# Performance work log

Hardware: AMD Instinct MI355X
Metric: run time of the kernel (lower is better)

The kernel has to match this reference:

```python
import jax, jax.numpy as jnp
import numpy as np

D_MODEL = 1024
BATCH = 8
SEQ = 2048
LN_EPS = 1e-5


def setup_inputs() -> dict:
    key = jax.random.key(0)
    ks = jax.random.split(key, 8)
    scale = 0.1 / np.sqrt(D_MODEL)
    x = jax.random.normal(ks[0], (BATCH, SEQ, D_MODEL), dtype=jnp.float32)
    return {
        "x": x,
        "ln_w": jnp.ones((D_MODEL,), jnp.float32),
        "ln_b": jnp.zeros((D_MODEL,), jnp.float32),
        # layer_idx=0, n_layers=4 -> ratio_1 = 1.0 (init), perturb slightly for a non-trivial mix
        "tmk": jnp.ones((D_MODEL,), jnp.float32) * 0.9,
        "tmv": jnp.ones((D_MODEL,), jnp.float32) * 0.9,
        "tmr": jnp.ones((D_MODEL,), jnp.float32) * 0.9,
        "decay_w": jnp.full((D_MODEL,), -0.5, jnp.float32)
        + 0.1 * jax.random.normal(ks[1], (D_MODEL,), jnp.float32),
        "Wk": scale * jax.random.normal(ks[2], (D_MODEL, D_MODEL), jnp.float32),
        "Wv": scale * jax.random.normal(ks[3], (D_MODEL, D_MODEL), jnp.float32),
        "Wr": scale * jax.random.normal(ks[4], (D_MODEL, D_MODEL), jnp.float32),
        "Wo": scale * jax.random.normal(ks[5], (D_MODEL, D_MODEL), jnp.float32),
    }


def _layernorm(z, w, b):
    m = jnp.mean(z, axis=-1, keepdims=True)
    v = jnp.mean(jnp.square(z - m), axis=-1, keepdims=True)
    return (z - m) * jax.lax.rsqrt(v + LN_EPS) * w + b


def reference(x, ln_w, ln_b, tmk, tmv, tmr, decay_w, Wk, Wv, Wr, Wo):
    # x: (B, T, D)
    xn = _layernorm(x, ln_w, ln_b)
    # prev_x at t=0 is zeros (not LN of zeros), afterwards LN(x_{t-1})
    prev = jnp.pad(xn[:, :-1, :], ((0, 0), (1, 0), (0, 0)))
    xk = xn * tmk + prev * (1.0 - tmk)
    xv = xn * tmv + prev * (1.0 - tmv)
    xr = xn * tmr + prev * (1.0 - tmr)
    k = jnp.einsum("btd,ed->bte", xk, Wk)
    v = jnp.einsum("btd,ed->bte", xv, Wv)
    r = jax.nn.sigmoid(jnp.einsum("btd,ed->bte", xr, Wr))
    decay = jax.nn.sigmoid(decay_w)  # (D,)

    kv = (k * v).swapaxes(0, 1)  # (T, B, D) time-major for scan

    def step(S, kv_t):
        S_new = decay * S + kv_t
        return S_new, S_new

    S0 = jnp.zeros((x.shape[0], x.shape[2]), x.dtype)
    final_S, S_seq = jax.lax.scan(step, S0, kv)
    S_seq = S_seq.swapaxes(0, 1)  # (B, T, D)

    out = x + r * jnp.einsum("btd,ed->bte", S_seq, Wo)
    return out, final_S, S_seq
```

## Files before the change

kernel.cpp:

```cpp
#include <hip/hip_runtime.h>
#include <cstdint>

#define D_MODEL 1024
#define SEQ 2048
#define BATCH 8
#define M_TOTAL (BATCH*SEQ)
#define NC 64
#define CL (SEQ/NC)

typedef float f32x4 __attribute__((ext_vector_type(4)));
typedef short bf16x8 __attribute__((ext_vector_type(8)));
typedef unsigned short u16x4 __attribute__((ext_vector_type(4)));

__device__ __forceinline__ float b2f(unsigned short s){
  union { float f; unsigned u; } z; z.u = ((unsigned)s) << 16; return z.f;
}
__device__ __forceinline__ unsigned short f2b(float f){
  union { float f; unsigned u; } z; z.f = f;
  unsigned u = z.u;
  u += 0x7fffu + ((u >> 16) & 1u);
  return (unsigned short)(u >> 16);
}
__device__ __forceinline__ float sigmoidf_(float v){
  return 1.0f / (1.0f + __expf(-v));
}
__device__ __forceinline__ void gld_lds16(const void* g, void* l){
  __builtin_amdgcn_global_load_lds((const __attribute__((address_space(1))) unsigned int*)g,
                                   (__attribute__((address_space(3))) unsigned int*)l,
                                   16, 0, 0);
}

__device__ __forceinline__ void swz256(int bid, int& m0, int& n0){
  int xcd = bid & 7;
  int loc = bid >> 3;
  int wg  = xcd*32 + loc;
  m0 = (wg >> 2) * 256;
  n0 = (wg & 3) * 256;
}

__global__ __launch_bounds__(256) void wconv_kernel(const float* __restrict__ W0, const float* __restrict__ W1,
                                                    const float* __restrict__ W2, const float* __restrict__ W3,
                                                    unsigned short* __restrict__ WC){
  int mat = blockIdx.y;
  const float* src = (mat==0) ? W0 : (mat==1) ? W1 : (mat==2) ? W2 : W3;
  size_t i = ((size_t)blockIdx.x*256 + threadIdx.x)*4;
  f32x4 v = *(const f32x4*)(src + i);
  u16x4 o; o[0]=f2b(v[0]); o[1]=f2b(v[1]); o[2]=f2b(v[2]); o[3]=f2b(v[3]);
  *(u16x4*)(WC + (size_t)mat*1048576 + i) = o;
}

__global__ __launch_bounds__(256) void lnmix_kernel(const float* __restrict__ x,
                                                    const float* __restrict__ lnw, const float* __restrict__ lnb,
                                                    const float* __restrict__ tmk, const float* __restrict__ tmv,
                                                    const float* __restrict__ tmr,
                                                    unsigned short* __restrict__ XK, unsigned short* __restrict__ XV,
                                                    unsigned short* __restrict__ XR){
  int m = blockIdx.x;
  int tid = threadIdx.x;
  bool first = (m & (SEQ-1)) == 0;
  size_t base = (size_t)m*D_MODEL + tid*4;
  f32x4 xc = *(const f32x4*)(x + base);
  f32x4 xp = {0.f,0.f,0.f,0.f};
  if (!first) xp = *(const f32x4*)(x + base - D_MODEL);

  float c1 = xc[0]+xc[1]+xc[2]+xc[3];
  float c2 = xc[0]*xc[0]+xc[1]*xc[1]+xc[2]*xc[2]+xc[3]*xc[3];
  float p1 = xp[0]+xp[1]+xp[2]+xp[3];
  float p2 = xp[0]*xp[0]+xp[1]*xp[1]+xp[2]*xp[2]+xp[3]*xp[3];
  #pragma unroll
  for (int off = 32; off > 0; off >>= 1){
    c1 += __shfl_xor(c1, off); c2 += __shfl_xor(c2, off);
    p1 += __shfl_xor(p1, off); p2 += __shfl_xor(p2, off);
  }
  __shared__ float rc1[4], rc2[4], rp1[4], rp2[4];
  int w = tid >> 6, lane = tid & 63;
  if (lane == 0){ rc1[w]=c1; rc2[w]=c2; rp1[w]=p1; rp2[w]=p2; }
  __syncthreads();
  c1 = rc1[0]+rc1[1]+rc1[2]+rc1[3];
  c2 = rc2[0]+rc2[1]+rc2[2]+rc2[3];
  p1 = rp1[0]+rp1[1]+rp1[2]+rp1[3];
  p2 = rp2[0]+rp2[1]+rp2[2]+rp2[3];
  float mC = c1*(1.0f/1024.0f), vC = c2*(1.0f/1024.0f)-mC*mC, rC = rsqrtf(vC+1e-5f);
  float mP = p1*(1.0f/1024.0f), vP = p2*(1.0f/1024.0f)-mP*mP, rP = rsqrtf(vP+1e-5f);

  f32x4 wv = *(const f32x4*)(lnw + tid*4);
  f32x4 bv = *(const f32x4*)(lnb + tid*4);
  f32x4 k4 = *(const f32x4*)(tmk + tid*4);
  f32x4 v4 = *(const f32x4*)(tmv + tid*4);
  f32x4 r4 = *(const f32x4*)(tmr + tid*4);
  u16x4 ok, ov, orr;
  #pragma unroll
  for (int j=0;j<4;j++){
    float nc = (xc[j]-mC)*rC*wv[j] + bv[j];
    float np = first ? 0.f : (xp[j]-mP)*rP*wv[j] + bv[j];
    ok[j]  = f2b(np + k4[j]*(nc-np));
    ov[j]  = f2b(np + v4[j]*(nc-np));
    orr[j] = f2b(np + r4[j]*(nc-np));
  }
  *(u16x4*)(XK + base) = ok;
  *(u16x4*)(XV + base) = ov;
  *(u16x4*)(XR + base) = orr;
}

__device__ __forceinline__ void gemm256_core(const unsigned short* __restrict__ A,
                                             const unsigned short* __restrict__ W,
                                             int m0, int n0, int tid,
                                             unsigned short* As, unsigned short* Bs,
                                             f32x4 (&acc)[8][4]){
  int wid = tid >> 6, lane = tid & 63;
  int wm = wid >> 2, wn = wid & 3;
  int fr = lane & 15, fg = lane >> 4;

  int offAg[4], offBg[4], offL[4];
  #pragma unroll
  for (int it = 0; it < 4; ++it){
    int chunk = it*512 + tid;
    int row = chunk >> 3;
    int cg = (chunk & 7) ^ (row & 7);
    offAg[it] = (m0+row)*D_MODEL + cg*8;
    offBg[it] = (n0+row)*D_MODEL + cg*8;
    offL[it]  = chunk*8;
  }

  #define STAGE(bsel, kt_) { \
    _Pragma("unroll") \
    for (int it = 0; it < 4; ++it){ \
      gld_lds16(A + offAg[it] + (kt_)*64, &As[(bsel)*16384 + offL[it]]); \
      gld_lds16(W + offBg[it] + (kt_)*64, &Bs[(bsel)*16384 + offL[it]]); \
    } }

  STAGE(0, 0);
  STAGE(1, 1);
  asm volatile("s_waitcnt vmcnt(8)" ::: "memory");
  __builtin_amdgcn_s_barrier();

  bf16x8 aL[4][2], aH[4][2], bL[2][2], bH[2][2];

  #pragma unroll 1
  for (int kt = 0; kt < 16; ++kt){
    const unsigned short* Ab = &As[(kt & 1)*16384];
    const unsigned short* Bb = &Bs[(kt & 1)*16384];

    #pragma unroll
    for (int mi=0; mi<4; ++mi)
      #pragma unroll
      for (int ks=0; ks<2; ++ks){
        int r = wm*128 + mi*16 + fr;
        aL[mi][ks] = *(const bf16x8*)(&Ab[r*64 + (((ks*4+fg)^(r&7))<<3)]);
      }
    #pragma unroll
    for (int ni=0; ni<2; ++ni)
      #pragma unroll
      for (int ks=0; ks<2; ++ks){
        int r = wn*64 + ni*16 + fr;
        bL[ni][ks] = *(const bf16x8*)(&Bb[r*64 + (((ks*4+fg)^(r&7))<<3)]);
      }
    __builtin_amdgcn_s_barrier();
    asm volatile("s_waitcnt lgkmcnt(0)" ::: "memory");
    __builtin_amdgcn_s_setprio(1);
    #pragma unroll
    for (int mi=0; mi<4; ++mi)
      #pragma unroll
      for (int ni=0; ni<2; ++ni)
        #pragma unroll
        for (int ks=0; ks<2; ++ks)
          acc[mi][ni] = __builtin_amdgcn_mfma_f32_16x16x32_bf16(aL[mi][ks], bL[ni][ks], acc[mi][ni], 0, 0, 0);
    __builtin_amdgcn_s_setprio(0);
    __builtin_amdgcn_s_barrier();

    #pragma unroll
    for (int ni=0; ni<2; ++ni)
      #pragma unroll
      for (int ks=0; ks<2; ++ks){
        int r = wn*64 + (ni+2)*16 + fr;
        bH[ni][ks] = *(const bf16x8*)(&Bb[r*64 + (((ks*4+fg)^(r&7))<<3)]);
      }
    __builtin_amdgcn_s_barrier();
    asm volatile("s_waitcnt lgkmcnt(0)" ::: "memory");
    __builtin_amdgcn_s_setprio(1);
    #pragma unroll
    for (int mi=0; mi<4; ++mi)
      #pragma unroll
      for (int ni=0; ni<2; ++ni)
        #pragma unroll
        for (int ks=0; ks<2; ++ks)
          acc[mi][ni+2] = __builtin_amdgcn_mfma_f32_16x16x32_bf16(aL[mi][ks], bH[ni][ks], acc[mi][ni+2], 0, 0, 0);
    __builtin_amdgcn_s_setprio(0);
    __builtin_amdgcn_s_barrier();

    #pragma unroll
    for (int mi=0; mi<4; ++mi)
      #pragma unroll
      for (int ks=0; ks<2; ++ks){
        int r = wm*128 + (mi+4)*16 + fr;
        aH[mi][ks] = *(const bf16x8*)(&Ab[r*64 + (((ks*4+fg)^(r&7))<<3)]);
      }
    asm volatile("s_waitcnt lgkmcnt(0)" ::: "memory");
    __builtin_amdgcn_s_barrier();
    asm volatile("" ::: "memory");
    __builtin_amdgcn_s_setprio(1);
    #pragma unroll
    for (int mi=0; mi<4; ++mi)
      #pragma unroll
      for (int ni=0; ni<2; ++ni)
        #pragma unroll
        for (int ks=0; ks<2; ++ks)
          acc[mi+4][ni+2] = __builtin_amdgcn_mfma_f32_16x16x32_bf16(aH[mi][ks], bH[ni][ks], acc[mi+4][ni+2], 0, 0, 0);
    __builtin_amdgcn_s_setprio(0);

    if (kt < 14) STAGE((kt & 1), kt+2);
    __builtin_amdgcn_s_setprio(1);
    #pragma unroll
    for (int mi=0; mi<4; ++mi)
      #pragma unroll
      for (int ni=0; ni<2; ++ni)
        #pragma unroll
        for (int ks=0; ks<2; ++ks)
          acc[mi+4][ni] = __builtin_amdgcn_mfma_f32_16x16x32_bf16(aH[mi][ks], bL[ni][ks], acc[mi+4][ni], 0, 0, 0);
    __builtin_amdgcn_s_setprio(0);
    if (kt < 14)      asm volatile("s_waitcnt vmcnt(8)" ::: "memory");
    else if (kt == 14) asm volatile("s_waitcnt vmcnt(0)" ::: "memory");
    if (kt < 15){
      __builtin_amdgcn_s_barrier();
      asm volatile("" ::: "memory");
    }
  }
  #undef STAGE
}

__global__ __launch_bounds__(512) void gemm_mix3_kernel(const unsigned short* __restrict__ XK,
                                                        const unsigned short* __restrict__ XV,
                                                        const unsigned short* __restrict__ XR,
                                                        const unsigned short* __restrict__ WC,
                                                        unsigned short* __restrict__ KB,
                                                        unsigned short* __restrict__ VB,
                                                        unsigned short* __restrict__ RB){
  __shared__ alignas(16) unsigned short As[2*16384];
  __shared__ alignas(16) unsigned short Bs[2*16384];
  int m0, n0; swz256(blockIdx.x, m0, n0);
  int z = blockIdx.z;
  int tid = threadIdx.x;
  const unsigned short* A = (z==0) ? XK : (z==1) ? XV : XR;
  const unsigned short* W = WC + (size_t)z*1048576;
  unsigned short* O       = (z==0) ? KB : (z==1) ? VB : RB;

  f32x4 acc[8][4];
  #pragma unroll
  for (int i=0;i<8;i++)
    #pragma unroll
    for (int j=0;j<4;j++){ acc[i][j][0]=0.f; acc[i][j][1]=0.f; acc[i][j][2]=0.f; acc[i][j][3]=0.f; }

  gemm256_core(A, W, m0, n0, tid, As, Bs, acc);

  int wid = tid >> 6, lane = tid & 63;
  int wm = wid >> 2, wn = wid & 3;
  int fr = lane & 15, fg = lane >> 4;
  #pragma unroll
  for (int mi=0; mi<8; ++mi){
    #pragma unroll
    for (int ni=0; ni<4; ++ni){
      int c = n0 + wn*64 + ni*16 + fr;
      #pragma unroll
      for (int j=0; j<4; ++j){
        int r = m0 + wm*128 + mi*16 + fg*4 + j;
        size_t idx = (size_t)r*D_MODEL + c;
        float val = acc[mi][ni][j];
        if (z == 2) val = sigmoidf_(val);
        O[idx] = f2b(val);
      }
    }
  }
}

__global__ __launch_bounds__(512) void gemm_out_kernel(const unsigned short* __restrict__ Sb,
                                                       const unsigned short* __restrict__ Wo,
                                                       const float* __restrict__ x,
                                                       const unsigned short* __restrict__ RB,
                                                       float* __restrict__ out){
  __shared__ alignas(16) unsigned short As[2*16384];
  __shared__ alignas(16) unsigned short Bs[2*16384];
  int m0, n0; swz256(blockIdx.x, m0, n0);
  int tid = threadIdx.x;

  f32x4 acc[8][4];
  #pragma unroll
  for (int i=0;i<8;i++)
    #pragma unroll
    for (int j=0;j<4;j++){ acc[i][j][0]=0.f; acc[i][j][1]=0.f; acc[i][j][2]=0.f; acc[i][j][3]=0.f; }

  gemm256_core(Sb, Wo, m0, n0, tid, As, Bs, acc);

  int wid = tid >> 6, lane = tid & 63;
  int wm = wid >> 2, wn = wid & 3;
  int fr = lane & 15, fg = lane >> 4;
  #pragma unroll
  for (int mi=0; mi<8; ++mi){
    #pragma unroll
    for (int ni=0; ni<4; ++ni){
      int c = n0 + wn*64 + ni*16 + fr;
      #pragma unroll
      for (int j=0; j<4; ++j){
        int r = m0 + wm*128 + mi*16 + fg*4 + j;
        size_t idx = (size_t)r*D_MODEL + c;
        float rr = b2f(RB[idx]);
        out[idx] = x[idx] + rr * acc[mi][ni][j];
      }
    }
  }
}

__global__ __launch_bounds__(256) void scan_p1_kernel(const unsigned short* __restrict__ kb,
                                                      const unsigned short* __restrict__ vb,
                                                      const float* __restrict__ dw,
                                                      float* __restrict__ carr){
  int bc = blockIdx.x;
  int b = bc >> 6, c = bc & (NC-1);
  int d0 = threadIdx.x * 4;
  float dx = sigmoidf_(dw[d0+0]);
  float dy = sigmoidf_(dw[d0+1]);
  float dz = sigmoidf_(dw[d0+2]);
  float dwv = sigmoidf_(dw[d0+3]);
  float Sx=0.f, Sy=0.f, Sz=0.f, Sw=0.f;
  size_t base = ((size_t)(b*SEQ + c*CL))*D_MODEL + d0;
  for (int i=0;i<CL;i++){
    u16x4 k4 = *(const u16x4*)(kb + base);
    u16x4 v4 = *(const u16x4*)(vb + base);
    Sx = dx*Sx + b2f(k4[0])*b2f(v4[0]);
    Sy = dy*Sy + b2f(k4[1])*b2f(v4[1]);
    Sz = dz*Sz + b2f(k4[2])*b2f(v4[2]);
    Sw = dwv*Sw + b2f(k4[3])*b2f(v4[3]);
    base += D_MODEL;
  }
  f32x4 o; o[0]=Sx; o[1]=Sy; o[2]=Sz; o[3]=Sw;
  *(f32x4*)(carr + (size_t)bc*D_MODEL + d0) = o;
}

__global__ __launch_bounds__(256) void scan_p2_kernel(const float* __restrict__ dw, float* __restrict__ carr){
  int gid = blockIdx.x*256 + threadIdx.x;
  int b = gid >> 10, d = gid & (D_MODEL-1);
  float dec = sigmoidf_(dw[d]);
  float dL = dec;
  #pragma unroll
  for (int i=0;i<5;i++) dL *= dL;
  float S = 0.f;
  for (int c=0;c<NC;c++){
    size_t idx = ((size_t)(b*NC + c))*D_MODEL + d;
    float cr = carr[idx];
    carr[idx] = S;
    S = dL*S + cr;
  }
}

__global__ __launch_bounds__(256) void scan_p3_kernel(const unsigned short* __restrict__ kb,
                                                      unsigned short* vsb,
                                                      const float* __restrict__ dw,
                                                      const float* __restrict__ cin,
                                                      float* __restrict__ sseq,
                                                      float* __restrict__ finalS){
  int bc = blockIdx.x;
  int b = bc >> 6, c = bc & (NC-1);
  int d0 = threadIdx.x * 4;
  float dx = sigmoidf_(dw[d0+0]);
  float dy = sigmoidf_(dw[d0+1]);
  float dz = sigmoidf_(dw[d0+2]);
  float dwv = sigmoidf_(dw[d0+3]);
  f32x4 S = *(const f32x4*)(cin + (size_t)bc*D_MODEL + d0);
  size_t base = ((size_t)(b*SEQ + c*CL))*D_MODEL + d0;
  for (int i=0;i<CL;i++){
    u16x4 k4 = *(const u16x4*)(kb + base);
    u16x4 v4 = *(const u16x4*)(vsb + base);
    S[0] = dx*S[0] + b2f(k4[0])*b2f(v4[0]);
    S[1] = dy*S[1] + b2f(k4[1])*b2f(v4[1]);
    S[2] = dz*S[2] + b2f(k4[2])*b2f(v4[2]);
    S[3] = dwv*S[3] + b2f(k4[3])*b2f(v4[3]);
    *(f32x4*)(sseq + base) = S;
    u16x4 s4; s4[0]=f2b(S[0]); s4[1]=f2b(S[1]); s4[2]=f2b(S[2]); s4[3]=f2b(S[3]);
    *(u16x4*)(vsb + base) = s4;
    base += D_MODEL;
  }
  if (c == NC-1)
    *(f32x4*)(finalS + (size_t)b*D_MODEL + d0) = S;
}

extern "C" void kernel_launch(void* const* d_in, const int* in_sizes, int n_in,
                              void* d_out, int out_size, void* d_ws, size_t ws_size,
                              hipStream_t stream){
  const float* x   = (const float*)d_in[0];
  const float* lnw = (const float*)d_in[1];
  const float* lnb = (const float*)d_in[2];
  const float* tmk = (const float*)d_in[3];
  const float* tmv = (const float*)d_in[4];
  const float* tmr = (const float*)d_in[5];
  const float* dw  = (const float*)d_in[6];
  const float* Wk  = (const float*)d_in[7];
  const float* Wv  = (const float*)d_in[8];
  const float* Wr  = (const float*)d_in[9];
  const float* Wo  = (const float*)d_in[10];

  float* out    = (float*)d_out;
  float* finalS = out + (size_t)M_TOTAL*D_MODEL;
  float* sseq   = finalS + (size_t)BATCH*D_MODEL;

  unsigned short* XK = (unsigned short*)d_out;
  unsigned short* XV = (unsigned short*)((char*)d_out + 33554432);
  unsigned short* XR = (unsigned short*)sseq;

  char* w = (char*)d_ws;
  unsigned short* WC   = (unsigned short*)(w + 0);
  unsigned short* VSB  = (unsigned short*)(w + 8388608);
  unsigned short* KB   = (unsigned short*)(w + 41943040);
  unsigned short* RB   = (unsigned short*)(w + 75497472);
  float*          CARR = (float*)(w + 109051904);

  wconv_kernel<<<dim3(1024,4), 256, 0, stream>>>(Wk, Wv, Wr, Wo, WC);
  lnmix_kernel<<<M_TOTAL, 256, 0, stream>>>(x, lnw, lnb, tmk, tmv, tmr, XK, XV, XR);

  gemm_mix3_kernel<<<dim3(256,1,3), 512, 0, stream>>>(XK, XV, XR, WC, KB, VSB, RB);

  scan_p1_kernel<<<BATCH*NC, 256, 0, stream>>>(KB, VSB, dw, CARR);
  scan_p2_kernel<<<32, 256, 0, stream>>>(dw, CARR);
  scan_p3_kernel<<<BATCH*NC, 256, 0, stream>>>(KB, VSB, dw, CARR, sseq, finalS);

  gemm_out_kernel<<<256, 512, 0, stream>>>(VSB, WC + (size_t)3*1048576, x, RB, out);
}
```

Before: 289.0 us.

## Fuse k*v product into V GEMM epilogue and batch 8 rows per LN block

```diff
diff --git a/kernel.cpp b/kernel.cpp
--- a/kernel.cpp
+++ b/kernel.cpp
@@ -55,51 +55,78 @@
                                                     const float* __restrict__ tmr,
                                                     unsigned short* __restrict__ XK, unsigned short* __restrict__ XV,
                                                     unsigned short* __restrict__ XR){
-  int m = blockIdx.x;
+  int r0 = blockIdx.x * 8;
   int tid = threadIdx.x;
-  bool first = (m & (SEQ-1)) == 0;
-  size_t base = (size_t)m*D_MODEL + tid*4;
-  f32x4 xc = *(const f32x4*)(x + base);
-  f32x4 xp = {0.f,0.f,0.f,0.f};
-  if (!first) xp = *(const f32x4*)(x + base - D_MODEL);
-
-  float c1 = xc[0]+xc[1]+xc[2]+xc[3];
-  float c2 = xc[0]*xc[0]+xc[1]*xc[1]+xc[2]*xc[2]+xc[3]*xc[3];
-  float p1 = xp[0]+xp[1]+xp[2]+xp[3];
-  float p2 = xp[0]*xp[0]+xp[1]*xp[1]+xp[2]*xp[2]+xp[3]*xp[3];
+  bool seqfirst = (r0 & (SEQ-1)) == 0;
+  size_t col = (size_t)tid*4;
+
+  f32x4 xr[9];
+  float s1[9], s2[9];
+  #pragma unroll
+  for (int i=0;i<9;i++){
+    if (i==0 && seqfirst){
+      xr[0][0]=0.f; xr[0][1]=0.f; xr[0][2]=0.f; xr[0][3]=0.f;
+    } else {
+      xr[i] = *(const f32x4*)(x + (size_t)(r0-1+i)*D_MODEL + col);
+    }
+    s1[i] = xr[i][0]+xr[i][1]+xr[i][2]+xr[i][3];
+    s2[i] = xr[i][0]*xr[i][0]+xr[i][1]*xr[i][1]+xr[i][2]*xr[i][2]+xr[i][3]*xr[i][3];
+  }
   #pragma unroll
   for (int off = 32; off > 0; off >>= 1){
-    c1 += __shfl_xor(c1, off); c2 += __shfl_xor(c2, off);
-    p1 += __shfl_xor(p1, off); p2 += __shfl_xor(p2, off);
-  }
-  __shared__ float rc1[4], rc2[4], rp1[4], rp2[4];
+    #pragma unroll
+    for (int i=0;i<9;i++){
+      s1[i] += __shfl_xor(s1[i], off);
+      s2[i] += __shfl_xor(s2[i], off);
+    }
+  }
+  __shared__ float red[4][18];
   int w = tid >> 6, lane = tid & 63;
-  if (lane == 0){ rc1[w]=c1; rc2[w]=c2; rp1[w]=p1; rp2[w]=p2; }
+  if (lane == 0){
+    #pragma unroll
+    for (int i=0;i<9;i++){ red[w][i]=s1[i]; red[w][9+i]=s2[i]; }
+  }
   __syncthreads();
-  c1 = rc1[0]+rc1[1]+rc1[2]+rc1[3];
-  c2 = rc2[0]+rc2[1]+rc2[2]+rc2[3];
-  p1 = rp1[0]+rp1[1]+rp1[2]+rp1[3];
-  p2 = rp2[0]+rp2[1]+rp2[2]+rp2[3];
-  float mC = c1*(1.0f/1024.0f), vC = c2*(1.0f/1024.0f)-mC*mC, rC = rsqrtf(vC+1e-5f);
-  float mP = p1*(1.0f/1024.0f), vP = p2*(1.0f/1024.0f)-mP*mP, rP = rsqrtf(vP+1e-5f);
-
-  f32x4 wv = *(const f32x4*)(lnw + tid*4);
-  f32x4 bv = *(const f32x4*)(lnb + tid*4);
-  f32x4 k4 = *(const f32x4*)(tmk + tid*4);
-  f32x4 v4 = *(const f32x4*)(tmv + tid*4);
-  f32x4 r4 = *(const f32x4*)(tmr + tid*4);
-  u16x4 ok, ov, orr;
-  #pragma unroll
-  for (int j=0;j<4;j++){
-    float nc = (xc[j]-mC)*rC*wv[j] + bv[j];
-    float np = first ? 0.f : (xp[j]-mP)*rP*wv[j] + bv[j];
-    ok[j]  = f2b(np + k4[j]*(nc-np));
-    ov[j]  = f2b(np + v4[j]*(nc-np));
-    orr[j] = f2b(np + r4[j]*(nc-np));
-  }
-  *(u16x4*)(XK + base) = ok;
-  *(u16x4*)(XV + base) = ov;
-  *(u16x4*)(XR + base) = orr;
+  float mean[9], rstd[9];
+  #pragma unroll
+  for (int i=0;i<9;i++){
+    float a = red[0][i]+red[1][i]+red[2][i]+red[3][i];
+    float b = red[0][9+i]+red[1][9+i]+red[2][9+i]+red[3][9+i];
+    mean[i] = a*(1.0f/1024.0f);
+    float var = b*(1.0f/1024.0f) - mean[i]*mean[i];
+    rstd[i] = rsqrtf(var + 1e-5f);
+  }
+
+  f32x4 wv = *(const f32x4*)(lnw + col);
+  f32x4 bv = *(const f32x4*)(lnb + col);
+  f32x4 k4 = *(const f32x4*)(tmk + col);
+  f32x4 v4 = *(const f32x4*)(tmv + col);
+  f32x4 r4 = *(const f32x4*)(tmr + col);
+
+  f32x4 np;
+  if (seqfirst){ np[0]=0.f; np[1]=0.f; np[2]=0.f; np[3]=0.f; }
+  else {
+    #pragma unroll
+    for (int j=0;j<4;j++) np[j] = (xr[0][j]-mean[0])*rstd[0]*wv[j] + bv[j];
+  }
+  #pragma unroll
+  for (int i=0;i<8;i++){
+    f32x4 nc;
+    #pragma unroll
+    for (int j=0;j<4;j++) nc[j] = (xr[i+1][j]-mean[i+1])*rstd[i+1]*wv[j] + bv[j];
+    u16x4 ok, ov, orr;
+    #pragma unroll
+    for (int j=0;j<4;j++){
+      ok[j]  = f2b(np[j] + k4[j]*(nc[j]-np[j]));
+      ov[j]  = f2b(np[j] + v4[j]*(nc[j]-np[j]));
+      orr[j] = f2b(np[j] + r4[j]*(nc[j]-np[j]));
+    }
+    size_t base = (size_t)(r0+i)*D_MODEL + col;
+    *(u16x4*)(XK + base) = ok;
+    *(u16x4*)(XV + base) = ov;
+    *(u16x4*)(XR + base) = orr;
+    np = nc;
+  }
 }
 
 __device__ __forceinline__ void gemm256_core(const unsigned short* __restrict__ A,
@@ -218,7 +245,7 @@
         for (int ks=0; ks<2; ++ks)
           acc[mi+4][ni] = __builtin_amdgcn_mfma_f32_16x16x32_bf16(aH[mi][ks], bL[ni][ks], acc[mi+4][ni], 0, 0, 0);
     __builtin_amdgcn_s_setprio(0);
-    if (kt < 14)      asm volatile("s_waitcnt vmcnt(8)" ::: "memory");
+    if (kt < 14)       asm volatile("s_waitcnt vmcnt(8)" ::: "memory");
     else if (kt == 14) asm volatile("s_waitcnt vmcnt(0)" ::: "memory");
     if (kt < 15){
       __builtin_amdgcn_s_barrier();
@@ -228,21 +255,20 @@
   #undef STAGE
 }
 
-__global__ __launch_bounds__(512) void gemm_mix3_kernel(const unsigned short* __restrict__ XK,
-                                                        const unsigned short* __restrict__ XV,
-                                                        const unsigned short* __restrict__ XR,
-                                                        const unsigned short* __restrict__ WC,
-                                                        unsigned short* __restrict__ KB,
-                                                        unsigned short* __restrict__ VB,
-                                                        unsigned short* __restrict__ RB){
+__global__ __launch_bounds__(512) void gemm_kr_kernel(const unsigned short* __restrict__ XK,
+                                                      const unsigned short* __restrict__ XR,
+                                                      const unsigned short* __restrict__ Wk,
+                                                      const unsigned short* __restrict__ Wr,
+                                                      unsigned short* __restrict__ KB,
+                                                      unsigned short* __restrict__ RB){
   __shared__ alignas(16) unsigned short As[2*16384];
   __shared__ alignas(16) unsigned short Bs[2*16384];
   int m0, n0; swz256(blockIdx.x, m0, n0);
   int z = blockIdx.z;
   int tid = threadIdx.x;
-  const unsigned short* A = (z==0) ? XK : (z==1) ? XV : XR;
-  const unsigned short* W = WC + (size_t)z*1048576;
-  unsigned short* O       = (z==0) ? KB : (z==1) ? VB : RB;
+  const unsigned short* A = z ? XR : XK;
+  const unsigned short* W = z ? Wr : Wk;
+  unsigned short* O       = z ? RB : KB;
 
   f32x4 acc[8][4];
   #pragma unroll
@@ -265,8 +291,42 @@
         int r = m0 + wm*128 + mi*16 + fg*4 + j;
         size_t idx = (size_t)r*D_MODEL + c;
         float val = acc[mi][ni][j];
-        if (z == 2) val = sigmoidf_(val);
+        if (z) val = sigmoidf_(val);
         O[idx] = f2b(val);
+      }
+    }
+  }
+}
+
+__global__ __launch_bounds__(512) void gemm_v_kernel(const unsigned short* __restrict__ XV,
+                                                     const unsigned short* __restrict__ Wv,
+                                                     unsigned short* __restrict__ KB){
+  __shared__ alignas(16) unsigned short As[2*16384];
+  __shared__ alignas(16) unsigned short Bs[2*16384];
+  int m0, n0; swz256(blockIdx.x, m0, n0);
+  int tid = threadIdx.x;
+
+  f32x4 acc[8][4];
+  #pragma unroll
+  for (int i=0;i<8;i++)
+    #pragma unroll
+    for (int j=0;j<4;j++){ acc[i][j][0]=0.f; acc[i][j][1]=0.f; acc[i][j][2]=0.f; acc[i][j][3]=0.f; }
+
+  gemm256_core(XV, Wv, m0, n0, tid, As, Bs, acc);
+
+  int wid = tid >> 6, lane = tid & 63;
+  int wm = wid >> 2, wn = wid & 3;
+  int fr = lane & 15, fg = lane >> 4;
+  #pragma unroll
+  for (int mi=0; mi<8; ++mi){
+    #pragma unroll
+    for (int ni=0; ni<4; ++ni){
+      int c = n0 + wn*64 + ni*16 + fr;
+      #pragma unroll
+      for (int j=0; j<4; ++j){
+        int r = m0 + wm*128 + mi*16 + fg*4 + j;
+        size_t idx = (size_t)r*D_MODEL + c;
+        KB[idx] = f2b(acc[mi][ni][j] * b2f(KB[idx]));
       }
     }
   }
@@ -309,8 +369,7 @@
   }
 }
 
-__global__ __launch_bounds__(256) void scan_p1_kernel(const unsigned short* __restrict__ kb,
-                                                      const unsigned short* __restrict__ vb,
+__global__ __launch_bounds__(256) void scan_p1_kernel(const unsigned short* __restrict__ kv,
                                                       const float* __restrict__ dw,
                                                       float* __restrict__ carr){
   int bc = blockIdx.x;
@@ -323,12 +382,11 @@
   float Sx=0.f, Sy=0.f, Sz=0.f, Sw=0.f;
   size_t base = ((size_t)(b*SEQ + c*CL))*D_MODEL + d0;
   for (int i=0;i<CL;i++){
-    u16x4 k4 = *(const u16x4*)(kb + base);
-    u16x4 v4 = *(const u16x4*)(vb + base);
-    Sx = dx*Sx + b2f(k4[0])*b2f(v4[0]);
-    Sy = dy*Sy + b2f(k4[1])*b2f(v4[1]);
-    Sz = dz*Sz + b2f(k4[2])*b2f(v4[2]);
-    Sw = dwv*Sw + b2f(k4[3])*b2f(v4[3]);
+    u16x4 k4 = *(const u16x4*)(kv + base);
+    Sx = dx*Sx + b2f(k4[0]);
+    Sy = dy*Sy + b2f(k4[1]);
+    Sz = dz*Sz + b2f(k4[2]);
+    Sw = dwv*Sw + b2f(k4[3]);
     base += D_MODEL;
   }
   f32x4 o; o[0]=Sx; o[1]=Sy; o[2]=Sz; o[3]=Sw;
@@ -351,12 +409,12 @@
   }
 }
 
-__global__ __launch_bounds__(256) void scan_p3_kernel(const unsigned short* __restrict__ kb,
-                                                      unsigned short* vsb,
+__global__ __launch_bounds__(256) void scan_p3_kernel(const unsigned short* __restrict__ kv,
                                                       const float* __restrict__ dw,
                                                       const float* __restrict__ cin,
                                                       float* __restrict__ sseq,
-                                                      float* __restrict__ finalS){
+                                                      float* __restrict__ finalS,
+                                                      unsigned short* __restrict__ sb16){
   int bc = blockIdx.x;
   int b = bc >> 6, c = bc & (NC-1);
   int d0 = threadIdx.x * 4;
@@ -367,15 +425,14 @@
   f32x4 S = *(const f32x4*)(cin + (size_t)bc*D_MODEL + d0);
   size_t base = ((size_t)(b*SEQ + c*CL))*D_MODEL + d0;
   for (int i=0;i<CL;i++){
-    u16x4 k4 = *(const u16x4*)(kb + base);
-    u16x4 v4 = *(const u16x4*)(vsb + base);
-    S[0] = dx*S[0] + b2f(k4[0])*b2f(v4[0]);
-    S[1] = dy*S[1] + b2f(k4[1])*b2f(v4[1]);
-    S[2] = dz*S[2] + b2f(k4[2])*b2f(v4[2]);
-    S[3] = dwv*S[3] + b2f(k4[3])*b2f(v4[3]);
+    u16x4 k4 = *(const u16x4*)(kv + base);
+    S[0] = dx*S[0] + b2f(k4[0]);
+    S[1] = dy*S[1] + b2f(k4[1]);
+    S[2] = dz*S[2] + b2f(k4[2]);
+    S[3] = dwv*S[3] + b2f(k4[3]);
     *(f32x4*)(sseq + base) = S;
     u16x4 s4; s4[0]=f2b(S[0]); s4[1]=f2b(S[1]); s4[2]=f2b(S[2]); s4[3]=f2b(S[3]);
-    *(u16x4*)(vsb + base) = s4;
+    *(u16x4*)(sb16 + base) = s4;
     base += D_MODEL;
   }
   if (c == NC-1)
@@ -407,19 +464,20 @@
 
   char* w = (char*)d_ws;
   unsigned short* WC   = (unsigned short*)(w + 0);
-  unsigned short* VSB  = (unsigned short*)(w + 8388608);
+  unsigned short* SB16 = (unsigned short*)(w + 8388608);
   unsigned short* KB   = (unsigned short*)(w + 41943040);
   unsigned short* RB   = (unsigned short*)(w + 75497472);
   float*          CARR = (float*)(w + 109051904);
 
   wconv_kernel<<<dim3(1024,4), 256, 0, stream>>>(Wk, Wv, Wr, Wo, WC);
-  lnmix_kernel<<<M_TOTAL, 256, 0, stream>>>(x, lnw, lnb, tmk, tmv, tmr, XK, XV, XR);
-
-  gemm_mix3_kernel<<<dim3(256,1,3), 512, 0, stream>>>(XK, XV, XR, WC, KB, VSB, RB);
-
-  scan_p1_kernel<<<BATCH*NC, 256, 0, stream>>>(KB, VSB, dw, CARR);
+  lnmix_kernel<<<M_TOTAL/8, 256, 0, stream>>>(x, lnw, lnb, tmk, tmv, tmr, XK, XV, XR);
+
+  gemm_kr_kernel<<<dim3(256,1,2), 512, 0, stream>>>(XK, XR, WC, WC + (size_t)2*1048576, KB, RB);
+  gemm_v_kernel<<<256, 512, 0, stream>>>(XV, WC + (size_t)1048576, KB);
+
+  scan_p1_kernel<<<BATCH*NC, 256, 0, stream>>>(KB, dw, CARR);
   scan_p2_kernel<<<32, 256, 0, stream>>>(dw, CARR);
-  scan_p3_kernel<<<BATCH*NC, 256, 0, stream>>>(KB, VSB, dw, CARR, sseq, finalS);
-
-  gemm_out_kernel<<<256, 512, 0, stream>>>(VSB, WC + (size_t)3*1048576, x, RB, out);
-}
+  scan_p3_kernel<<<BATCH*NC, 256, 0, stream>>>(KB, dw, CARR, sseq, finalS, SB16);
+
+  gemm_out_kernel<<<256, 512, 0, stream>>>(SB16, WC + (size_t)3*1048576, x, RB, out);
+}
```

Result: faster. 266.1 us (-7.9%).
